# Performance work log

Measured on AMD Instinct MI355X. Metric: run time of the kernel, lower is better.

## Reference

```python
import jax, jax.numpy as jnp
import numpy as np

EMBED_DIM = 1024
NUM_HEADS = 16


def _mha(q_in, k_in, v_in, w_in, b_in, w_out, b_out, num_heads, mask=None):
    """torch.nn.MultiheadAttention (batch_first=True) forward, dropout=0.
    q_in: [B, Lq, E], k_in/v_in: [B, Lk, E].
    w_in: [3E, E], b_in: [3E], w_out: [E, E], b_out: [E].
    """
    E = q_in.shape[-1]
    hd = E // num_heads
    wq, wk, wv = jnp.split(w_in, 3, axis=0)
    bq, bk, bv = jnp.split(b_in, 3)
    q = q_in @ wq.T + bq
    k = k_in @ wk.T + bk
    v = v_in @ wv.T + bv
    B, Lq = q.shape[0], q.shape[1]
    Lk = k.shape[1]
    q = q.reshape(B, Lq, num_heads, hd)
    k = k.reshape(B, Lk, num_heads, hd)
    v = v.reshape(B, Lk, num_heads, hd)
    scale = 1.0 / jnp.sqrt(jnp.asarray(hd, dtype=q.dtype))
    scores = jnp.einsum('bqhd,bkhd->bhqk', q, k) * scale  # [B,H,Lq,Lk]
    if mask is not None:
        scores = scores + mask  # additive mask, broadcast over B,H
    attn = jax.nn.softmax(scores, axis=-1)
    out = jnp.einsum('bhqk,bkhd->bqhd', attn, v).reshape(B, Lq, E)
    return out @ w_out.T + b_out


def setup_inputs() -> dict:
    key = jax.random.key(0)
    ks = jax.random.split(key, 20)
    B, T, S, P, E = 4, 1024, 16, 256, EMBED_DIM
    std = 0.02
    inp = {
        'text_tokens': jax.random.normal(ks[0], (B, T, E), jnp.float32),
        'patch_groups': jax.random.normal(ks[1], (S, B, P, E), jnp.float32),
        'cls_tokens': jax.random.normal(ks[2], (B, S, E), jnp.float32),
        'int_token': jax.random.normal(ks[3], (B, 1, E), jnp.float32),
    }
    for i, name in enumerate(['text', 'patch', 'int']):
        inp[f'{name}_w_in'] = jax.random.normal(ks[4 + 4 * i], (3 * E, E), jnp.float32) * std
        inp[f'{name}_b_in'] = jnp.zeros((3 * E,), jnp.float32)
        inp[f'{name}_w_out'] = jax.random.normal(ks[5 + 4 * i], (E, E), jnp.float32) * std
        inp[f'{name}_b_out'] = jnp.zeros((E,), jnp.float32)
    return inp


def reference(text_tokens, patch_groups, cls_tokens, int_token,
              text_w_in, text_b_in, text_w_out, text_b_out,
              patch_w_in, patch_b_in, patch_w_out, patch_b_out,
              int_w_in, int_b_in, int_w_out, int_b_out):
    H = NUM_HEADS
    T = text_tokens.shape[1]
    # causal text self-attention
    causal = jnp.triu(jnp.full((T, T), -jnp.inf, dtype=text_tokens.dtype), k=1)
    text_out = _mha(text_tokens, text_tokens, text_tokens,
                    text_w_in, text_b_in, text_w_out, text_b_out, H, mask=causal)

    # per-stroke block-diagonal patch self-attention (vmapped over strokes)
    patch_self = jax.vmap(lambda p: _mha(p, p, p, patch_w_in, patch_b_in,
                                         patch_w_out, patch_b_out, H))
    patch_outs = patch_self(patch_groups)  # [S, B, P, E]

    # per-stroke CLS cross-attention over its patches (same weights)
    cls_q = jnp.swapaxes(cls_tokens, 0, 1)[:, :, None, :]  # [S, B, 1, E]
    cls_cross = jax.vmap(lambda c, p: _mha(c, p, p, patch_w_in, patch_b_in,
                                           patch_w_out, patch_b_out, H))
    cls_out = cls_cross(cls_q, patch_groups)  # [S, B, 1, E]
    cls_out = jnp.swapaxes(cls_out[:, :, 0, :], 0, 1)  # [B, S, E]

    # global INT cross-attention over [text_out ; cls_out]
    context = jnp.concatenate([text_out, cls_out], axis=1)
    int_out = _mha(int_token, context, context,
                   int_w_in, int_b_in, int_w_out, int_b_out, H)
    return (text_out, patch_outs, cls_out, int_out)
```

## Files before the change

### kernel.cpp

```cpp
#include <hip/hip_runtime.h>

typedef unsigned short u16;
typedef unsigned int u32;
typedef __attribute__((ext_vector_type(8))) short short8;
typedef __attribute__((ext_vector_type(4))) float floatx4;

#define EDIM 1024
#define H3   3072
#define HD   64

__device__ __forceinline__ float bf2f(u16 u) {
    union { u32 i; float f; } x; x.i = ((u32)u) << 16; return x.f;
}
__device__ __forceinline__ u16 f2bf(float f) {
    u32 u = __float_as_uint(f);
    u32 r = u + 0x7fffu + ((u >> 16) & 1u);
    return (u16)(r >> 16);
}

__global__ void detect_dtype(const u16* __restrict__ t, int* __restrict__ flag)
{
    __shared__ int cnt;
    if (threadIdx.x == 0) cnt = 0;
    __syncthreads();
    u16 u = t[threadIdx.x * 2];
    int e = (u >> 7) & 0xFF;
    int ok = (u == 0) || (e >= 108 && e <= 136);
    atomicAdd(&cnt, ok);
    __syncthreads();
    if (threadIdx.x == 0) flag[0] = (cnt >= 128) ? 1 : 0;
}

__global__ __launch_bounds__(256) void to_bf16_2(
    const void* __restrict__ sa, u16* __restrict__ da, int na8,
    const void* __restrict__ sb, u16* __restrict__ db, int nb8,
    const int* __restrict__ flag)
{
    int idx = blockIdx.x * 256 + threadIdx.x;
    const void* s; u16* d; long off;
    if (idx < na8) {
        s = sa; d = da; off = (long)idx * 8;
    } else {
        idx -= na8;
        if (idx >= nb8) return;
        s = sb; d = db; off = (long)idx * 8;
    }
    if (flag[0]) {
        *(uint4*)(d + off) = *(const uint4*)((const u16*)s + off);
    } else {
        const float* f = (const float*)s + off;
        float4 f0 = *(const float4*)f;
        float4 f1 = *(const float4*)(f + 4);
        uint4 p;
        p.x = (u32)f2bf(f0.x) | ((u32)f2bf(f0.y) << 16);
        p.y = (u32)f2bf(f0.z) | ((u32)f2bf(f0.w) << 16);
        p.z = (u32)f2bf(f1.x) | ((u32)f2bf(f1.y) << 16);
        p.w = (u32)f2bf(f1.z) | ((u32)f2bf(f1.w) << 16);
        *(uint4*)(d + off) = p;
    }
}

__global__ __launch_bounds__(256) void gemm_bt_bias(
    const u16* __restrict__ A, const u16* __restrict__ W,
    const u16* __restrict__ bias, u16* __restrict__ C,
    int M, int N, int K, int w_row0, int b_off)
{
    __shared__ u16 sA[128 * 64];
    __shared__ u16 sB[128 * 64];
    const int tid  = threadIdx.x;
    const int wave = tid >> 6, lane = tid & 63;

    const int MT = (M + 127) >> 7, NT = N >> 7;
    const int tpg = NT * 8;
    const int grp = blockIdx.x / tpg;
    const int rem = blockIdx.x - grp * tpg;
    int gsz = MT - grp * 8; if (gsz > 8) gsz = 8;
    const int mt = grp * 8 + rem % gsz;
    const int nt = rem / gsz;
    const int m0 = mt * 128, n0 = nt * 128;

    const int wm = (wave & 1) * 64, wn = (wave >> 1) * 64;
    const int r16 = lane & 15, q8 = (lane >> 4) * 8;
    const int lrow = lane >> 3, lcol = (lane & 7) * 8;

    floatx4 acc[4][4];
#pragma unroll
    for (int i = 0; i < 4; ++i)
#pragma unroll
        for (int j = 0; j < 4; ++j)
            acc[i][j] = (floatx4){0.f, 0.f, 0.f, 0.f};

    const u16* Wb = W + (size_t)w_row0 * K;
    for (int k0 = 0; k0 < K; k0 += 64) {
#pragma unroll
        for (int t = 0; t < 4; ++t) {
            int rr = wave * 32 + t * 8;
            int ga = m0 + rr + lrow; if (ga > M - 1) ga = M - 1;
            __builtin_amdgcn_global_load_lds(
                (const __attribute__((address_space(1))) void*)(A + (size_t)ga * K + k0 + lcol),
                (__attribute__((address_space(3))) void*)&sA[rr * 64], 16, 0, 0);
            int gb = n0 + rr + lrow; if (gb > N - 1) gb = N - 1;
            __builtin_amdgcn_global_load_lds(
                (const __attribute__((address_space(1))) void*)(Wb + (size_t)gb * K + k0 + lcol),
                (__attribute__((address_space(3))) void*)&sB[rr * 64], 16, 0, 0);
        }
        __syncthreads();
#pragma unroll
        for (int kk = 0; kk < 64; kk += 32) {
            short8 af[4], bg[4];
#pragma unroll
            for (int i = 0; i < 4; ++i)
                af[i] = *(const short8*)&sA[(wm + 16 * i + r16) * 64 + kk + q8];
#pragma unroll
            for (int j = 0; j < 4; ++j)
                bg[j] = *(const short8*)&sB[(wn + 16 * j + r16) * 64 + kk + q8];
#pragma unroll
            for (int i = 0; i < 4; ++i)
#pragma unroll
                for (int j = 0; j < 4; ++j)
                    acc[i][j] = __builtin_amdgcn_mfma_f32_16x16x32_bf16(
                        af[i], bg[j], acc[i][j], 0, 0, 0);
        }
        __syncthreads();
    }

#pragma unroll
    for (int j = 0; j < 4; ++j) {
        int col = n0 + wn + 16 * j + r16;
        float bv = bf2f(bias[b_off + col]);
#pragma unroll
        for (int i = 0; i < 4; ++i) {
            int rowb = m0 + wm + 16 * i + (lane >> 4) * 4;
#pragma unroll
            for (int r = 0; r < 4; ++r) {
                int row = rowb + r;
                if (row < M)
                    C[(size_t)row * N + col] = f2bf(acc[i][j][r] + bv);
            }
        }
    }
}

__global__ __launch_bounds__(256) void attn_flash(
    const u16* __restrict__ qkv, u16* __restrict__ out, int L, int causal)
{
    __shared__ u16 sK[64 * 64];
    __shared__ u16 sVt[64 * 64];
    __shared__ u16 sP[4 * 16 * 64];
    const int tid = threadIdx.x;
    const int wave = tid >> 6, lane = tid & 63;
    const int h = blockIdx.y, g = blockIdx.z, qt = blockIdx.x;
    const size_t grow0 = (size_t)g * L;
    const int qw0 = qt * 64 + wave * 16;
    const int r16 = lane & 15, q8 = (lane >> 4) * 8;

    short8 qf0, qf1;
    {
        const u16* qp = qkv + (grow0 + qw0 + r16) * (size_t)H3 + h * HD + q8;
        qf0 = *(const short8*)qp;
        qf1 = *(const short8*)(qp + 32);
    }

    floatx4 o_acc[4];
#pragma unroll
    for (int dg = 0; dg < 4; ++dg) o_acc[dg] = (floatx4){0.f, 0.f, 0.f, 0.f};
    float m_r[4], l_r[4];
#pragma unroll
    for (int r = 0; r < 4; ++r) { m_r[r] = -3.0e38f; l_r[r] = 0.f; }

    u16* sPw = sP + wave * 1024;
    const int nch = causal ? (qt + 1) : (L >> 6);

    for (int c = 0; c < nch; ++c) {
        const int k0 = c * 64;
        __syncthreads();
#pragma unroll
        for (int t = 0; t < 2; ++t) {
            int idx = t * 256 + tid;
            int r = idx >> 3, c8 = (idx & 7) * 8;
            const u16* kp = qkv + (grow0 + k0 + r) * (size_t)H3 + EDIM + h * HD + c8;
            *(uint4*)&sK[r * 64 + c8] = *(const uint4*)kp;
            uint4 vw = *(const uint4*)(kp + EDIM);
            u32 vu[4] = {vw.x, vw.y, vw.z, vw.w};
#pragma unroll
            for (int i = 0; i < 4; ++i) {
                sVt[(c8 + 2 * i) * 64 + r]     = (u16)(vu[i] & 0xffffu);
                sVt[(c8 + 2 * i + 1) * 64 + r] = (u16)(vu[i] >> 16);
            }
        }
        __syncthreads();

        float sc[4][4];
#pragma unroll
        for (int kg = 0; kg < 4; ++kg) {
            const u16* kb = &sK[(kg * 16 + r16) * 64];
            short8 kf0 = *(const short8*)(kb + q8);
            short8 kf1 = *(const short8*)(kb + 32 + q8);
            floatx4 a = (floatx4){0.f, 0.f, 0.f, 0.f};
            a = __builtin_amdgcn_mfma_f32_16x16x32_bf16(qf0, kf0, a, 0, 0, 0);
            a = __builtin_amdgcn_mfma_f32_16x16x32_bf16(qf1, kf1, a, 0, 0, 0);
#pragma unroll
            for (int r = 0; r < 4; ++r) sc[kg][r] = a[r] * 0.125f;
        }
        const bool domask = causal && (k0 + 63 > qw0);
        if (domask) {
#pragma unroll
            for (int kg = 0; kg < 4; ++kg)
#pragma unroll
                for (int r = 0; r < 4; ++r) {
                    int key = k0 + kg * 16 + r16;
                    int qg  = qw0 + (lane >> 4) * 4 + r;
                    if (key > qg) sc[kg][r] = -3.0e38f;
                }
        }
        float rmax[4];
#pragma unroll
        for (int r = 0; r < 4; ++r)
            rmax[r] = fmaxf(fmaxf(sc[0][r], sc[1][r]), fmaxf(sc[2][r], sc[3][r]));
#pragma unroll
        for (int m = 1; m <= 8; m <<= 1)
#pragma unroll
            for (int r = 0; r < 4; ++r)
                rmax[r] = fmaxf(rmax[r], __shfl_xor(rmax[r], m));
        float alpha[4], rsum[4];
#pragma unroll
        for (int r = 0; r < 4; ++r) {
            float mn = fmaxf(m_r[r], rmax[r]);
            alpha[r] = __expf(m_r[r] - mn);
            m_r[r] = mn; rsum[r] = 0.f;
        }
#pragma unroll
        for (int kg = 0; kg < 4; ++kg)
#pragma unroll
            for (int r = 0; r < 4; ++r) {
                float p = __expf(sc[kg][r] - m_r[r]);
                rsum[r] += p;
                sPw[((lane >> 4) * 4 + r) * 64 + kg * 16 + r16] = f2bf(p);
            }
#pragma unroll
        for (int m = 1; m <= 8; m <<= 1)
#pragma unroll
            for (int r = 0; r < 4; ++r)
                rsum[r] += __shfl_xor(rsum[r], m);
#pragma unroll
        for (int r = 0; r < 4; ++r) l_r[r] = l_r[r] * alpha[r] + rsum[r];
#pragma unroll
        for (int dg = 0; dg < 4; ++dg)
#pragma unroll
            for (int r = 0; r < 4; ++r) o_acc[dg][r] *= alpha[r];

        __asm__ volatile("" ::: "memory");

#pragma unroll
        for (int kc = 0; kc < 2; ++kc) {
            short8 pf = *(const short8*)&sPw[r16 * 64 + kc * 32 + q8];
#pragma unroll
            for (int dg = 0; dg < 4; ++dg) {
                short8 vf = *(const short8*)&sVt[(dg * 16 + r16) * 64 + kc * 32 + q8];
                o_acc[dg] = __builtin_amdgcn_mfma_f32_16x16x32_bf16(pf, vf, o_acc[dg], 0, 0, 0);
            }
        }
    }

    float inv[4];
#pragma unroll
    for (int r = 0; r < 4; ++r) inv[r] = 1.f / l_r[r];
#pragma unroll
    for (int dg = 0; dg < 4; ++dg)
#pragma unroll
        for (int r = 0; r < 4; ++r) {
            int q = qw0 + (lane >> 4) * 4 + r;
            out[(grow0 + q) * (size_t)EDIM + h * HD + dg * 16 + r16] =
                f2bf(o_acc[dg][r] * inv[r]);
        }
}

__global__ __launch_bounds__(64) void attn_cross(
    const u16* __restrict__ kv, const u16* __restrict__ qv,
    u16* __restrict__ out, int mode)
{
    const int h = blockIdx.x, gi = blockIdx.y, lane = threadIdx.x;
    int Lk, kvStride, kOff, vOff, qRow;
    size_t kvRow0;
    if (mode == 0) {
        Lk = 256; kvStride = H3; kOff = EDIM; vOff = 2 * EDIM;
        kvRow0 = (size_t)gi * 256;
        int s = gi >> 2, b = gi & 3;
        qRow = b * 16 + s;
    } else {
        Lk = 1040; kvStride = 2 * EDIM; kOff = 0; vOff = EDIM;
        kvRow0 = (size_t)gi * 1040;
        qRow = gi;
    }
    __shared__ float sq[64];
    __shared__ float sp[1040];
    sq[lane] = bf2f(qv[(size_t)qRow * EDIM + h * HD + lane]);
    __syncthreads();

    const int nt = (Lk + 63) >> 6;
    float mloc = -3.0e38f;
    for (int t = 0; t < nt; ++t) {
        int j = t * 64 + lane;
        if (j < Lk) {
            const uint4* kp = (const uint4*)(kv + (kvRow0 + j) * (size_t)kvStride + kOff + h * HD);
            float a0 = 0, a1 = 0;
#pragma unroll
            for (int tt = 0; tt < 8; ++tt) {
                uint4 w = kp[tt];
                u32 u[4] = {w.x, w.y, w.z, w.w};
#pragma unroll
                for (int i = 0; i < 4; ++i) {
                    a0 += sq[tt * 8 + i * 2]     * bf2f((u16)(u[i] & 0xffffu));
                    a1 += sq[tt * 8 + i * 2 + 1] * bf2f((u16)(u[i] >> 16));
                }
            }
            float s_ = (a0 + a1) * 0.125f;
            sp[j] = s_;
            mloc = fmaxf(mloc, s_);
        }
    }
#pragma unroll
    for (int off = 32; off; off >>= 1) mloc = fmaxf(mloc, __shfl_xor(mloc, off));
    float lsum = 0.f;
    for (int t = 0; t < nt; ++t) {
        int j = t * 64 + lane;
        if (j < Lk) { float p = __expf(sp[j] - mloc); sp[j] = p; lsum += p; }
    }
#pragma unroll
    for (int off = 32; off; off >>= 1) lsum += __shfl_xor(lsum, off);
    __syncthreads();

    float o = 0.f;
    for (int j = 0; j < Lk; ++j)
        o += sp[j] * bf2f(kv[(kvRow0 + j) * (size_t)kvStride + vOff + h * HD + lane]);
    out[(size_t)qRow * EDIM + h * HD + lane] = f2bf(o / lsum);
}

__global__ __launch_bounds__(256) void build_ctx(
    const u16* __restrict__ to, const u16* __restrict__ co, u16* __restrict__ ctx)
{
    int idx = blockIdx.x * 256 + threadIdx.x;
    int row = idx >> 7, c8 = (idx & 127) << 3;
    int b = row / 1040, t = row - b * 1040;
    const u16* src = (t < 1024)
        ? (to + ((size_t)(b * 1024 + t) * EDIM + c8))
        : (co + ((size_t)(b * 16 + (t - 1024)) * EDIM + c8));
    *(uint4*)(ctx + (size_t)row * EDIM + c8) = *(const uint4*)src;
}

__global__ __launch_bounds__(256) void emit_out(
    const u16* __restrict__ src, void* __restrict__ dst, int n8,
    const int* __restrict__ flag)
{
    int idx = blockIdx.x * 256 + threadIdx.x;
    if (idx >= n8) return;
    const u16* s = src + (size_t)idx * 8;
    if (flag[0]) {
        *(uint4*)((u16*)dst + (size_t)idx * 8) = *(const uint4*)s;
    } else {
        float4 f0, f1;
        f0.x = bf2f(s[0]); f0.y = bf2f(s[1]); f0.z = bf2f(s[2]); f0.w = bf2f(s[3]);
        f1.x = bf2f(s[4]); f1.y = bf2f(s[5]); f1.z = bf2f(s[6]); f1.w = bf2f(s[7]);
        float4* dp = (float4*)dst + (size_t)idx * 2;
        dp[0] = f0; dp[1] = f1;
    }
}

extern "C" void kernel_launch(void* const* d_in, const int* in_sizes, int n_in,
                              void* d_out, int out_size, void* d_ws, size_t ws_size,
                              hipStream_t stream)
{
    const void* text  = d_in[0];
    const void* patch = d_in[1];
    const void* cls   = d_in[2];
    const void* intok = d_in[3];
    const void* t_win  = d_in[4];  const void* t_bin  = d_in[5];
    const void* t_wout = d_in[6];  const void* t_bout = d_in[7];
    const void* p_win  = d_in[8];  const void* p_bin  = d_in[9];
    const void* p_wout = d_in[10]; const void* p_bout = d_in[11];
    const void* i_win  = d_in[12]; const void* i_bin  = d_in[13];
    const void* i_wout = d_in[14]; const void* i_bout = d_in[15];

    u16* ws = (u16*)d_ws;
    int* flag       = (int*)d_ws;
    u16* qkv_text   = ws + 64;
    u16* qkv_patch  = ws + 12582976;
    u16* attn_text  = ws + 62914624;
    u16* attn_patch = ws + 67108928;
    u16* cls_q      = ws + 83886144;
    u16* attn_cls   = ws + 83951680;

    u16* text_bf  = attn_text;
    u16* patch_bf = attn_patch;
    u16* cls_bf   = attn_cls;
    u16* int_bf   = cls_q;
    u16* WT   = qkv_patch;
    u16* WTb  = WT + 3145728;
    u16* WP   = attn_text;
    u16* WPb  = WP + 3145728;
    u16* WO1  = qkv_text;
    u16* WO1b = WO1 + 1048576;
    u16* WO2  = qkv_text + 1049600;
    u16* WO2b = WO2 + 1048576;
    u16* WI   = qkv_text + 4259840;
    u16* WIb  = WI + 3145728;
    u16* WIO  = qkv_text + 7408640;
    u16* WIOb = WIO + 1048576;
    u16* ctx      = qkv_text;
    u16* kv_int   = qkv_patch;
    u16* q_int    = qkv_patch + 8519680;
    u16* attn_int = qkv_patch + 8523776;
    u16* out_ws   = qkv_patch + 8527872;
    u16* to_ws = out_ws;
    u16* po_ws = out_ws + 4194304;
    u16* co_ws = out_ws + 20971520;
    u16* io_ws = out_ws + 21037056;

    dim3 blk(256);
    detect_dtype<<<1, blk, 0, stream>>>((const u16*)text, flag);

    to_bf16_2<<<dim3(10240), blk, 0, stream>>>(text, text_bf, 524288,
                                               patch, patch_bf, 2097152, flag);
    to_bf16_2<<<dim3(32), blk, 0, stream>>>(cls, cls_bf, 8192, cls, cls_bf, 0, flag);
    to_bf16_2<<<dim3(1538), blk, 0, stream>>>(t_win, WT, 393216, t_bin, WTb, 384, flag);

    gemm_bt_bias<<<dim3(32 * 24), blk, 0, stream>>>(text_bf, WT, WTb, qkv_text,
                                                    4096, 3072, 1024, 0, 0);
    to_bf16_2<<<dim3(1538), blk, 0, stream>>>(p_win, WP, 393216, p_bin, WPb, 384, flag);
    gemm_bt_bias<<<dim3(128 * 24), blk, 0, stream>>>(patch_bf, WP, WPb, qkv_patch,
                                                     16384, 3072, 1024, 0, 0);
    gemm_bt_bias<<<dim3(1 * 8), blk, 0, stream>>>(cls_bf, WP, WPb, cls_q,
                                                  64, 1024, 1024, 0, 0);

    attn_flash<<<dim3(16, 16, 4), blk, 0, stream>>>(qkv_text, attn_text, 1024, 1);
    attn_flash<<<dim3(4, 16, 64), blk, 0, stream>>>(qkv_patch, attn_patch, 256, 0);
    attn_cross<<<dim3(16, 64), dim3(64), 0, stream>>>(qkv_patch, cls_q, attn_cls, 0);

    to_bf16_2<<<dim3(513), blk, 0, stream>>>(t_wout, WO1, 131072, t_bout, WO1b, 128, flag);
    to_bf16_2<<<dim3(513), blk, 0, stream>>>(p_wout, WO2, 131072, p_bout, WO2b, 128, flag);
    to_bf16_2<<<dim3(1538), blk, 0, stream>>>(i_win, WI, 393216, i_bin, WIb, 384, flag);
    to_bf16_2<<<dim3(513), blk, 0, stream>>>(i_wout, WIO, 131072, i_bout, WIOb, 128, flag);

    gemm_bt_bias<<<dim3(32 * 8), blk, 0, stream>>>(attn_text, WO1, WO1b, to_ws,
                                                   4096, 1024, 1024, 0, 0);
    gemm_bt_bias<<<dim3(128 * 8), blk, 0, stream>>>(attn_patch, WO2, WO2b, po_ws,
                                                    16384, 1024, 1024, 0, 0);
    gemm_bt_bias<<<dim3(1 * 8), blk, 0, stream>>>(attn_cls, WO2, WO2b, co_ws,
                                                  64, 1024, 1024, 0, 0);

    build_ctx<<<dim3(2080), blk, 0, stream>>>(to_ws, co_ws, ctx);
    gemm_bt_bias<<<dim3(33 * 16), blk, 0, stream>>>(ctx, WI, WIb, kv_int,
                                                    4160, 2048, 1024, 1024, 1024);
    to_bf16_2<<<dim3(2), blk, 0, stream>>>(intok, int_bf, 512, intok, int_bf, 0, flag);
    gemm_bt_bias<<<dim3(1 * 8), blk, 0, stream>>>(int_bf, WI, WIb, q_int,
                                                  4, 1024, 1024, 0, 0);
    attn_cross<<<dim3(16, 4), dim3(64), 0, stream>>>(kv_int, q_int, attn_int, 1);
    gemm_bt_bias<<<dim3(1 * 8), blk, 0, stream>>>(attn_int, WIO, WIOb, io_ws,
                                                  4, 1024, 1024, 0, 0);

    emit_out<<<dim3(10274), blk, 0, stream>>>(out_ws, d_out, 2630144, flag);
}
```

Measured before the change: 1.005 ms.

## Add 256x256-tile triple-buffered GEMM with direct global-to-LDS loads for large projections

Adds a new gemm256 kernel with 512 threads, 256x256 output tiles, a three-slot LDS ring filled by global_load_lds, XOR-swizzled LDS reads, grouped tile ordering for L2 reuse, and split-phase MFMA with setprio. It replaces the older 128-tile GEMM for the big QKV, patch output and INT KV projections. The aim is more data reuse per tile and overlap of loads with MFMA work. The cost is heavy register pressure from 32 accumulators, and fewer blocks on the smaller GEMMs (136 blocks for the INT projection) can leave CUs underused. Edge rows are handled by clamping the load row index.

Result: faster. 956.7 us (-4.8%).

```diff
diff --git a/kernel.cpp b/kernel.cpp
--- a/kernel.cpp
+++ b/kernel.cpp
@@ -131,6 +131,147 @@
 #pragma unroll
         for (int i = 0; i < 4; ++i) {
             int rowb = m0 + wm + 16 * i + (lane >> 4) * 4;
+#pragma unroll
+            for (int r = 0; r < 4; ++r) {
+                int row = rowb + r;
+                if (row < M)
+                    C[(size_t)row * N + col] = f2bf(acc[i][j][r] + bv);
+            }
+        }
+    }
+}
+
+#define SLOT_U16 16384
+
+__device__ __forceinline__ void stage_one(
+    const u16* __restrict__ G, int gbase, int gmax, int K, int k2,
+    const u16* ldsdst, int lane)
+{
+    int mm = lane ^ (lane >> 3);
+    int gr = gbase + (mm >> 2); if (gr > gmax) gr = gmax;
+    __builtin_amdgcn_global_load_lds(
+        (const __attribute__((address_space(1))) void*)(G + (size_t)gr * K + k2 + (mm & 3) * 8),
+        (__attribute__((address_space(3))) void*)ldsdst, 16, 0, 0);
+}
+
+__global__ __launch_bounds__(512, 2) void gemm256(
+    const u16* __restrict__ A, const u16* __restrict__ W,
+    const u16* __restrict__ bias, u16* __restrict__ C,
+    int M, int N, int K, int w_row0, int b_off)
+{
+    __shared__ u16 lds[3 * SLOT_U16];
+    const int tid = threadIdx.x;
+    const int wid = tid >> 6, lane = tid & 63;
+
+    const int MT = (M + 255) >> 8, NT = N >> 8;
+    const int tpg = NT * 8;
+    const int grp = blockIdx.x / tpg;
+    const int rem = blockIdx.x - grp * tpg;
+    int gsz = MT - grp * 8; if (gsz > 8) gsz = 8;
+    const int mt = grp * 8 + rem % gsz;
+    const int nt = rem / gsz;
+    const int m0 = mt << 8, n0 = nt << 8;
+
+    const int wmB = (wid >> 2) * 128;
+    const int wnB = (wid & 3) * 64;
+    const int r16 = lane & 15, q8 = (lane >> 4) * 8;
+    const int w16 = wid * 16;
+    const u16* Wb = W + (size_t)w_row0 * K;
+
+    floatx4 acc[8][4];
+#pragma unroll
+    for (int i = 0; i < 8; ++i)
+#pragma unroll
+        for (int j = 0; j < 4; ++j)
+            acc[i][j] = (floatx4){0.f, 0.f, 0.f, 0.f};
+
+    const int KT = K >> 5;
+
+#pragma unroll
+    for (int t = 0; t < 2; ++t) {
+        const int k2 = t << 5;
+        const u16* sl = lds + t * SLOT_U16;
+        stage_one(A,  m0 + w16,       M - 1, K, k2, sl + w16 * 32, lane);
+        stage_one(A,  m0 + 128 + w16, M - 1, K, k2, sl + (128 + w16) * 32, lane);
+        stage_one(Wb, n0 + w16,       N - 1, K, k2, sl + 8192 + w16 * 32, lane);
+        stage_one(Wb, n0 + 128 + w16, N - 1, K, k2, sl + 8192 + (128 + w16) * 32, lane);
+    }
+    asm volatile("s_waitcnt vmcnt(4)" ::: "memory");
+    __builtin_amdgcn_s_barrier();
+
+    for (int t = 0; t < KT; ++t) {
+        const int slot = t % 3;
+        const u16* sAc = lds + slot * SLOT_U16;
+        const u16* sBc = sAc + 8192;
+        const int t2 = t + 2;
+        const u16* sl2 = lds + (t2 % 3) * SLOT_U16;
+        const int k2 = t2 << 5;
+        const bool dost = t2 < KT;
+
+        short8 bg[4];
+        short8 af0[4];
+#pragma unroll
+        for (int i = 0; i < 4; ++i) {
+            int ar = wmB + i * 16 + r16;
+            int off = ar * 32 + q8;
+            af0[i] = *(const short8*)&sAc[off ^ ((((u32)off >> 6) & 7) << 3)];
+        }
+#pragma unroll
+        for (int j = 0; j < 4; ++j) {
+            int br = wnB + j * 16 + r16;
+            int off = br * 32 + q8;
+            bg[j] = *(const short8*)&sBc[off ^ ((((u32)off >> 6) & 7) << 3)];
+        }
+        if (dost) {
+            stage_one(A, m0 + w16,       M - 1, K, k2, sl2 + w16 * 32, lane);
+            stage_one(A, m0 + 128 + w16, M - 1, K, k2, sl2 + (128 + w16) * 32, lane);
+        }
+        __builtin_amdgcn_s_barrier();
+        __builtin_amdgcn_s_setprio(1);
+#pragma unroll
+        for (int i = 0; i < 4; ++i)
+#pragma unroll
+            for (int j = 0; j < 4; ++j)
+                acc[i][j] = __builtin_amdgcn_mfma_f32_16x16x32_bf16(
+                    af0[i], bg[j], acc[i][j], 0, 0, 0);
+        __builtin_amdgcn_s_setprio(0);
+        __builtin_amdgcn_s_barrier();
+
+        short8 af1[4];
+#pragma unroll
+        for (int i = 0; i < 4; ++i) {
+            int ar = wmB + 64 + i * 16 + r16;
+            int off = ar * 32 + q8;
+            af1[i] = *(const short8*)&sAc[off ^ ((((u32)off >> 6) & 7) << 3)];
+        }
+        if (dost) {
+            stage_one(Wb, n0 + w16,       N - 1, K, k2, sl2 + 8192 + w16 * 32, lane);
+            stage_one(Wb, n0 + 128 + w16, N - 1, K, k2, sl2 + 8192 + (128 + w16) * 32, lane);
+        }
+        __builtin_amdgcn_s_barrier();
+        __builtin_amdgcn_s_setprio(1);
+#pragma unroll
+        for (int i = 0; i < 4; ++i)
+#pragma unroll
+            for (int j = 0; j < 4; ++j)
+                acc[4 + i][j] = __builtin_amdgcn_mfma_f32_16x16x32_bf16(
+                    af1[i], bg[j], acc[4 + i][j], 0, 0, 0);
+        __builtin_amdgcn_s_setprio(0);
+
+        if (t < KT - 1) {
+            if (t == KT - 2) asm volatile("s_waitcnt vmcnt(0)" ::: "memory");
+            else             asm volatile("s_waitcnt vmcnt(4)" ::: "memory");
+            __builtin_amdgcn_s_barrier();
+        }
+    }
+
+#pragma unroll
+    for (int j = 0; j < 4; ++j) {
+        int col = n0 + wnB + j * 16 + r16;
+        float bv = bf2f(bias[b_off + col]);
+#pragma unroll
+        for (int i = 0; i < 8; ++i) {
+            int rowb = m0 + wmB + i * 16 + (lane >> 4) * 4;
 #pragma unroll
             for (int r = 0; r < 4; ++r) {
                 int row = rowb + r;
@@ -417,6 +558,7 @@
     u16* io_ws = out_ws + 21037056;
 
     dim3 blk(256);
+    dim3 blk5(512);
     detect_dtype<<<1, blk, 0, stream>>>((const u16*)text, flag);
 
     to_bf16_2<<<dim3(10240), blk, 0, stream>>>(text, text_bf, 524288,
@@ -424,11 +566,11 @@
     to_bf16_2<<<dim3(32), blk, 0, stream>>>(cls, cls_bf, 8192, cls, cls_bf, 0, flag);
     to_bf16_2<<<dim3(1538), blk, 0, stream>>>(t_win, WT, 393216, t_bin, WTb, 384, flag);
 
-    gemm_bt_bias<<<dim3(32 * 24), blk, 0, stream>>>(text_bf, WT, WTb, qkv_text,
-                                                    4096, 3072, 1024, 0, 0);
+    gemm256<<<dim3(192), blk5, 0, stream>>>(text_bf, WT, WTb, qkv_text,
+                                            4096, 3072, 1024, 0, 0);
     to_bf16_2<<<dim3(1538), blk, 0, stream>>>(p_win, WP, 393216, p_bin, WPb, 384, flag);
-    gemm_bt_bias<<<dim3(128 * 24), blk, 0, stream>>>(patch_bf, WP, WPb, qkv_patch,
-                                                     16384, 3072, 1024, 0, 0);
+    gemm256<<<dim3(768), blk5, 0, stream>>>(patch_bf, WP, WPb, qkv_patch,
+                                            16384, 3072, 1024, 0, 0);
     gemm_bt_bias<<<dim3(1 * 8), blk, 0, stream>>>(cls_bf, WP, WPb, cls_q,
                                                   64, 1024, 1024, 0, 0);
 
@@ -443,14 +585,14 @@
 
     gemm_bt_bias<<<dim3(32 * 8), blk, 0, stream>>>(attn_text, WO1, WO1b, to_ws,
                                                    4096, 1024, 1024, 0, 0);
-    gemm_bt_bias<<<dim3(128 * 8), blk, 0, stream>>>(attn_patch, WO2, WO2b, po_ws,
-                                                    16384, 1024, 1024, 0, 0);
+    gemm256<<<dim3(256), blk5, 0, stream>>>(attn_patch, WO2, WO2b, po_ws,
+                                            16384, 1024, 1024, 0, 0);
     gemm_bt_bias<<<dim3(1 * 8), blk, 0, stream>>>(attn_cls, WO2, WO2b, co_ws,
                                                   64, 1024, 1024, 0, 0);
 
     build_ctx<<<dim3(2080), blk, 0, stream>>>(to_ws, co_ws, ctx);
-    gemm_bt_bias<<<dim3(33 * 16), blk, 0, stream>>>(ctx, WI, WIb, kv_int,
-                                                    4160, 2048, 1024, 1024, 1024);
+    gemm256<<<dim3(136), blk5, 0, stream>>>(ctx, WI, WIb, kv_int,
+                                            4160, 2048, 1024, 1024, 1024);
     to_bf16_2<<<dim3(2), blk, 0, stream>>>(intok, int_bf, 512, intok, int_bf, 0, flag);
     gemm_bt_bias<<<dim3(1 * 8), blk, 0, stream>>>(int_bf, WI, WIb, q_int,
                                                   4, 1024, 1024, 0, 0);
```
